# Optimization experiments

Measured on AMD Instinct MI355X. Metric: run time of the kernel, lower is better.

Reference implementation:

```python
import jax, jax.numpy as jnp
import numpy as np

M = 8          # ensemble size
B = 16384      # batch
HIST = 5       # history
L = 384        # latent_dim
A = 1          # action_dim
HID = 512      # hidden_dim
NHL = 2        # num_hidden_layers
DIN = L * HIST + A * HIST  # 1925
EPS = 1e-5     # BatchNorm eps


def setup_inputs() -> dict:
    key = jax.random.key(0)
    ks = jax.random.split(key, 6)
    w = lambda k, shape: (jax.random.normal(k, shape, jnp.float32) * 0.02)
    return {
        "z_hist": jax.random.normal(ks[0], (B, HIST, L), jnp.float32),
        "a_hist": jax.random.normal(ks[1], (B, HIST, A), jnp.float32),
        # per-model parameters, stacked along leading ensemble dim M
        "W1": w(ks[2], (M, DIN, HID)),
        "b1": jnp.zeros((M, HID), jnp.float32),
        "Wh": w(ks[3], (NHL, M, HID, HID)),
        "bh": jnp.zeros((NHL, M, HID), jnp.float32),
        "gamma": jnp.ones((NHL, M, HID), jnp.float32),
        "beta": jnp.zeros((NHL, M, HID), jnp.float32),
        "rmean": jnp.zeros((NHL, M, HID), jnp.float32),   # BN running mean (eval mode)
        "rvar": jnp.ones((NHL, M, HID), jnp.float32),      # BN running var (eval mode)
        "W3": w(ks[4], (M, HID, L)),
        "b3": jnp.zeros((M, L), jnp.float32),
    }


def reference(z_hist, a_hist, W1, b1, Wh, bh, gamma, beta, rmean, rvar, W3, b3):
    # EnsembleTransitionModel.forward, batched over the ensemble dim instead of
    # a Python loop over models. BatchNorm in eval mode; Dropout inactive (eval).
    bsz = z_hist.shape[0]
    x = jnp.concatenate([z_hist.reshape(bsz, -1), a_hist.reshape(bsz, -1)], axis=1)  # [B, DIN]
    # input projection + ReLU: [M, B, HID]
    h = jax.nn.relu(jnp.einsum('bi,mih->mbh', x, W1) + b1[:, None, :])
    n_layers = Wh.shape[0]
    for l in range(n_layers):  # small fixed structural loop (num_hidden_layers)
        h = jnp.einsum('mbh,mhk->mbk', h, Wh[l]) + bh[l][:, None, :]
        h = (h - rmean[l][:, None, :]) * jax.lax.rsqrt(rvar[l][:, None, :] + EPS)
        h = jax.nn.relu(h * gamma[l][:, None, :] + beta[l][:, None, :])
    delta = jnp.einsum('mbh,mhl->mbl', h, W3) + b3[:, None, :]
    # residual: pred_z = z_t + delta, broadcast over ensemble dim
    return delta + z_hist[:, -1, :][None, :, :]
```

## Files before the change

kernel.cpp:

```cpp
#include <hip/hip_runtime.h>
#include <hip/hip_bf16.h>

#define M_ENS 8
#define BATCH 16384
#define HIST 5
#define LDIM 384
#define HID 512
#define NHL 2
#define DIN 1925
#define KP 2048

typedef unsigned short u16;
typedef unsigned int u32;
typedef __attribute__((ext_vector_type(8))) short bf16x8;
typedef __attribute__((ext_vector_type(4))) float f32x4;

__device__ __forceinline__ u16 f2b(float f) {
    u32 u = __builtin_bit_cast(u32, f);
    u32 r = (u + 0x7fffu + ((u >> 16) & 1u)) >> 16;
    return (u16)r;
}

__global__ void build_x(const float* __restrict__ z, const float* __restrict__ a,
                        u16* __restrict__ xp) {
    int idx = blockIdx.x * 256 + threadIdx.x;
    int b = idx / (KP / 2);
    int k2 = (idx % (KP / 2)) * 2;
    if (b >= BATCH) return;
    u32 packed = 0;
#pragma unroll
    for (int j = 0; j < 2; ++j) {
        int k = k2 + j;
        float v = 0.f;
        if (k < HIST * LDIM) v = z[(size_t)b * (HIST * LDIM) + k];
        else if (k < DIN)    v = a[b * HIST + (k - HIST * LDIM)];
        packed |= ((u32)f2b(v)) << (16 * j);
    }
    *(u32*)(&xp[(size_t)b * KP + k2]) = packed;
}

__global__ void transpose_cvt(const float* __restrict__ in, u16* __restrict__ out,
                              int R, int C, int Rp) {
    __shared__ float tile[32][33];
    const float* inb = in + (size_t)blockIdx.z * R * C;
    u16* outb = out + (size_t)blockIdx.z * C * Rp;
    int r0 = blockIdx.x * 32, c0 = blockIdx.y * 32;
    int tx = threadIdx.x & 31, ty = threadIdx.x >> 5;
#pragma unroll
    for (int i = 0; i < 32; i += 8) {
        int r = r0 + ty + i;
        float v = 0.f;
        if (r < R) v = inb[(size_t)r * C + c0 + tx];
        tile[ty + i][tx] = v;
    }
    __syncthreads();
#pragma unroll
    for (int i = 0; i < 32; i += 8) {
        outb[(size_t)(c0 + ty + i) * Rp + r0 + tx] = f2b(tile[tx][ty + i]);
    }
}

__global__ void make_tables(const float* __restrict__ bh, const float* __restrict__ gamma,
                            const float* __restrict__ beta, const float* __restrict__ rmean,
                            const float* __restrict__ rvar, float* __restrict__ s,
                            float* __restrict__ t, int n) {
    int i = blockIdx.x * 256 + threadIdx.x;
    if (i >= n) return;
    float inv = rsqrtf(rvar[i] + 1e-5f);
    float sc = gamma[i] * inv;
    s[i] = sc;
    t[i] = (bh[i] - rmean[i]) * sc + beta[i];
}

#define BARRIER asm volatile("s_barrier" ::: "memory")

template <int MODE>
__global__ __launch_bounds__(512, 2) void gemm8p(
    const u16* __restrict__ A, const u16* __restrict__ Bw,
    const float* __restrict__ Sv, const float* __restrict__ Tv,
    u16* __restrict__ Ho, int K) {
    extern __shared__ char smem[];
    const int tid = threadIdx.x;
    const int lane = tid & 63;
    const int wid = tid >> 6;
    const int wm = wid >> 2;
    const int wn = wid & 3;

    const int nwg = gridDim.x;
    const int swz = (blockIdx.x & 7) * (nwg >> 3) + (blockIdx.x >> 3);

    int rowT, colT, mI;
    const u16 *Ab, *Bb;
    int lda, ldb;
    if (MODE == 0) {
        rowT = swz >> 4; colT = swz & 15;
        Ab = A; lda = KP;
        Bb = Bw + (size_t)colT * 256 * KP; ldb = KP;
        mI = 0;
    } else {
        mI = swz >> 7;
        int rem = swz & 127;
        rowT = rem >> 1; colT = rem & 1;
        Ab = A + (size_t)mI * BATCH * HID; lda = HID;
        Bb = Bw + (size_t)mI * HID * HID + (size_t)colT * 256 * HID; ldb = HID;
    }
    const int rowBase = rowT * 256;
    const int NT = K >> 6;

    auto STAGE = [&](int par, int op, int half, int tk) {
#pragma unroll
        for (int i = 0; i < 2; ++i) {
            int ii = wid * 2 + i;
            int row = ii * 8 + (lane >> 3);
            int gc = lane & 7;
            const u16* src;
            if (op == 0)
                src = Ab + (size_t)(rowBase + half * 128 + row) * lda + tk * 64 + ((gc ^ (row & 7)) << 3);
            else
                src = Bb + (size_t)(half * 128 + row) * ldb + tk * 64 + ((gc ^ (row & 7)) << 3);
            u16* dst = (u16*)(smem + par * 65536 + op * 32768 + half * 16384) + (size_t)(ii * 64 + lane) * 8;
            __builtin_amdgcn_global_load_lds((const __attribute__((address_space(1))) void*)src,
                                             (__attribute__((address_space(3))) void*)dst, 16, 0, 0);
        }
    };

    const int laneRow = lane & 15;
    int xg[2];
    xg[0] = (((lane >> 4)) ^ (lane & 7)) << 4;
    xg[1] = ((4 | (lane >> 4)) ^ (lane & 7)) << 4;
#define RDF(base, r, kk) (*(const bf16x8*)((base) + (size_t)(r) * 128 + xg[kk]))

    f32x4 acc[8][4] = {};
    bf16x8 af[4][2], bfr[4][2];
    const int bcol0 = (wn & 1) * 64;

    STAGE(0, 1, 0, 0); STAGE(0, 1, 1, 0);
    STAGE(0, 0, 0, 0); STAGE(0, 0, 1, 0);
    if (NT > 1) { STAGE(1, 1, 0, 1); STAGE(1, 1, 1, 1); }
    asm volatile("s_waitcnt vmcnt(4)" ::: "memory");
    BARRIER;

    for (int T = 0; T < NT; ++T) {
        const int p = T & 1;
        const char* pA = smem + p * 65536 + wm * 16384;
        const char* pB = smem + p * 65536 + 32768 + (wn >> 1) * 16384;

#pragma unroll
        for (int mf = 0; mf < 4; ++mf) {
            af[mf][0] = RDF(pA, mf * 16 + laneRow, 0);
            af[mf][1] = RDF(pA, mf * 16 + laneRow, 1);
        }
#pragma unroll
        for (int nf = 0; nf < 2; ++nf) {
            bfr[nf][0] = RDF(pB, bcol0 + nf * 16 + laneRow, 0);
            bfr[nf][1] = RDF(pB, bcol0 + nf * 16 + laneRow, 1);
        }
        if (T + 1 < NT) STAGE((T + 1) & 1, 0, 0, T + 1);
        BARRIER;
        __builtin_amdgcn_s_setprio(1);
#pragma unroll
        for (int kk = 0; kk < 2; ++kk)
#pragma unroll
            for (int mf = 0; mf < 4; ++mf)
#pragma unroll
                for (int nf = 0; nf < 2; ++nf)
                    acc[mf][nf] = __builtin_amdgcn_mfma_f32_16x16x32_bf16(af[mf][kk], bfr[nf][kk], acc[mf][nf], 0, 0, 0);
        __builtin_amdgcn_s_setprio(0);
        BARRIER;

#pragma unroll
        for (int nf = 2; nf < 4; ++nf) {
            bfr[nf][0] = RDF(pB, bcol0 + nf * 16 + laneRow, 0);
            bfr[nf][1] = RDF(pB, bcol0 + nf * 16 + laneRow, 1);
        }
        if (T + 1 < NT) STAGE((T + 1) & 1, 0, 1, T + 1);
        BARRIER;
        __builtin_amdgcn_s_setprio(1);
#pragma unroll
        for (int kk = 0; kk < 2; ++kk)
#pragma unroll
            for (int mf = 0; mf < 4; ++mf)
#pragma unroll
                for (int nf = 2; nf < 4; ++nf)
                    acc[mf][nf] = __builtin_amdgcn_mfma_f32_16x16x32_bf16(af[mf][kk], bfr[nf][kk], acc[mf][nf], 0, 0, 0);
        __builtin_amdgcn_s_setprio(0);
        BARRIER;

#pragma unroll
        for (int mf = 0; mf < 4; ++mf) {
            af[mf][0] = RDF(pA, (4 + mf) * 16 + laneRow, 0);
            af[mf][1] = RDF(pA, (4 + mf) * 16 + laneRow, 1);
        }
        if (T + 2 < NT) STAGE(p, 1, 0, T + 2);
        BARRIER;
        __builtin_amdgcn_s_setprio(1);
#pragma unroll
        for (int kk = 0; kk < 2; ++kk)
#pragma unroll
            for (int mf = 0; mf < 4; ++mf)
#pragma unroll
                for (int nf = 2; nf < 4; ++nf)
                    acc[4 + mf][nf] = __builtin_amdgcn_mfma_f32_16x16x32_bf16(af[mf][kk], bfr[nf][kk], acc[4 + mf][nf], 0, 0, 0);
        __builtin_amdgcn_s_setprio(0);
        BARRIER;

        if (T + 2 < NT) {
            STAGE(p, 1, 1, T + 2);
            asm volatile("s_waitcnt vmcnt(4)" ::: "memory");
        } else {
            asm volatile("s_waitcnt vmcnt(0)" ::: "memory");
        }
        BARRIER;
        __builtin_amdgcn_s_setprio(1);
#pragma unroll
        for (int kk = 0; kk < 2; ++kk)
#pragma unroll
            for (int mf = 0; mf < 4; ++mf)
#pragma unroll
                for (int nf = 0; nf < 2; ++nf)
                    acc[4 + mf][nf] = __builtin_amdgcn_mfma_f32_16x16x32_bf16(af[mf][kk], bfr[nf][kk], acc[4 + mf][nf], 0, 0, 0);
        __builtin_amdgcn_s_setprio(0);
        BARRIER;
    }

#pragma unroll
    for (int mf = 0; mf < 8; ++mf) {
        int row = rowBase + wm * 128 + mf * 16 + ((lane >> 4) << 2);
#pragma unroll
        for (int nf = 0; nf < 4; ++nf) {
            int c = colT * 256 + wn * 64 + nf * 16 + (lane & 15);
            if (MODE == 0) {
                float tb = Tv[c];
                size_t base = (size_t)(c >> 9) * BATCH * HID + (c & 511);
#pragma unroll
                for (int q = 0; q < 4; ++q) {
                    float v = acc[mf][nf][q] + tb;
                    Ho[base + (size_t)(row + q) * HID] = f2b(v > 0.f ? v : 0.f);
                }
            } else {
                float sc = Sv[mI * HID + c], tb = Tv[mI * HID + c];
                u16* H = Ho + (size_t)mI * BATCH * HID;
#pragma unroll
                for (int q = 0; q < 4; ++q) {
                    float v = acc[mf][nf][q] * sc + tb;
                    H[(size_t)(row + q) * HID + c] = f2b(v > 0.f ? v : 0.f);
                }
            }
        }
    }
}

template <int MODE>
__global__ __launch_bounds__(256, 2) void gemm_bt(
    const u16* __restrict__ A, size_t aStride, int lda,
    const u16* __restrict__ Bt, size_t bStride,
    const float* __restrict__ Sv, const float* __restrict__ Tv, int ptStride,
    u16* __restrict__ Ho, size_t hStride,
    float* __restrict__ Fo, size_t fStride,
    const float* __restrict__ Zres,
    int K, int m0) {
    __shared__ u16 As[128 * 64];
    __shared__ u16 Bs[128 * 64];

    const int tid = threadIdx.x;
    const int lane = tid & 63;
    const int wid = tid >> 6;
    const int wr = (wid >> 1) * 64;
    const int wc = (wid & 1) * 64;
    const int z = blockIdx.z;
    const int rowBase = blockIdx.x * 128;
    const int colBase = blockIdx.y * 128;

    const u16* Ab = A + (size_t)z * aStride;
    const u16* Bb = Bt + (size_t)z * bStride;

    f32x4 acc[4][4] = {};

    int aoff[4], boff[4];
#pragma unroll
    for (int f = 0; f < 4; ++f) {
        int ar = wr + f * 16 + (lane & 15);
        aoff[f] = (ar * 128 + ((lane >> 4) * 16)) ^ ((ar & 7) << 4);
        int br = wc + f * 16 + (lane & 15);
        boff[f] = (br * 128 + ((lane >> 4) * 16)) ^ ((br & 7) << 4);
    }

    for (int k0 = 0; k0 < K; k0 += 64) {
#pragma unroll
        for (int i = 0; i < 4; ++i) {
            int gg = i * 256 + tid;
            int row = gg >> 3, gc = gg & 7;
            const u16* srcA = Ab + (size_t)(rowBase + row) * lda + k0 + ((gc ^ (row & 7)) << 3);
            __builtin_amdgcn_global_load_lds(
                (const __attribute__((address_space(1))) void*)srcA,
                (__attribute__((address_space(3))) void*)(As + gg * 8), 16, 0, 0);
            const u16* srcB = Bb + (size_t)(colBase + row) * K + k0 + ((gc ^ (row & 7)) << 3);
            __builtin_amdgcn_global_load_lds(
                (const __attribute__((address_space(1))) void*)srcB,
                (__attribute__((address_space(3))) void*)(Bs + gg * 8), 16, 0, 0);
        }
        __syncthreads();
#pragma unroll
        for (int kk = 0; kk < 2; ++kk) {
            bf16x8 af[4], bfr[4];
#pragma unroll
            for (int f = 0; f < 4; ++f) {
                af[f]  = *(const bf16x8*)((const char*)As + (aoff[f] ^ (kk << 6)));
                bfr[f] = *(const bf16x8*)((const char*)Bs + (boff[f] ^ (kk << 6)));
            }
#pragma unroll
            for (int i = 0; i < 4; ++i)
#pragma unroll
                for (int j = 0; j < 4; ++j)
                    acc[i][j] = __builtin_amdgcn_mfma_f32_16x16x32_bf16(af[i], bfr[j], acc[i][j], 0, 0, 0);
        }
        __syncthreads();
    }

    const int mg = m0 + z;
#pragma unroll
    for (int i = 0; i < 4; ++i) {
        int rbase = rowBase + wr + i * 16 + ((lane >> 4) << 2);
#pragma unroll
        for (int j = 0; j < 4; ++j) {
            int n = colBase + wc + j * 16 + (lane & 15);
            if (MODE == 0) {
                float bias = Tv[(size_t)mg * ptStride + n];
                u16* H = Ho + (size_t)z * hStride;
#pragma unroll
                for (int q = 0; q < 4; ++q) {
                    float v = acc[i][j][q] + bias;
                    v = v > 0.f ? v : 0.f;
                    H[(size_t)(rbase + q) * HID + n] = f2b(v);
                }
            } else if (MODE == 1) {
                float sc = Sv[(size_t)mg * ptStride + n];
                float tt = Tv[(size_t)mg * ptStride + n];
                u16* H = Ho + (size_t)z * hStride;
#pragma unroll
                for (int q = 0; q < 4; ++q) {
                    float v = acc[i][j][q] * sc + tt;
                    v = v > 0.f ? v : 0.f;
                    H[(size_t)(rbase + q) * HID + n] = f2b(v);
                }
            } else {
                float bias = Tv[(size_t)mg * ptStride + n];
                float* F = Fo + (size_t)z * fStride;
#pragma unroll
                for (int q = 0; q < 4; ++q) {
                    int b = rbase + q;
                    float v = acc[i][j][q] + bias + Zres[(size_t)b * (HIST * LDIM) + (HIST - 1) * LDIM + n];
                    F[(size_t)b * LDIM + n] = v;
                }
            }
        }
    }
}

extern "C" void kernel_launch(void* const* d_in, const int* in_sizes, int n_in,
                              void* d_out, int out_size, void* d_ws, size_t ws_size,
                              hipStream_t stream) {
    const float* z_hist = (const float*)d_in[0];
    const float* a_hist = (const float*)d_in[1];
    const float* W1    = (const float*)d_in[2];
    const float* b1    = (const float*)d_in[3];
    const float* Wh    = (const float*)d_in[4];
    const float* bh    = (const float*)d_in[5];
    const float* gamma = (const float*)d_in[6];
    const float* beta  = (const float*)d_in[7];
    const float* rmean = (const float*)d_in[8];
    const float* rvar  = (const float*)d_in[9];
    const float* W3    = (const float*)d_in[10];
    const float* b3    = (const float*)d_in[11];
    float* out = (float*)d_out;

    char* ws = (char*)d_ws;
    size_t off = 0;
    auto alloc = [&](size_t bytes) {
        void* p = ws + off;
        off = (off + bytes + 255) & ~(size_t)255;
        return p;
    };
    u16* xp  = (u16*)alloc((size_t)BATCH * KP * 2);
    u16* W1t = (u16*)alloc((size_t)M_ENS * HID * KP * 2);
    u16* Wht = (u16*)alloc((size_t)NHL * M_ENS * HID * HID * 2);
    u16* W3t = (u16*)alloc((size_t)M_ENS * LDIM * HID * 2);
    float* stab = (float*)alloc((size_t)NHL * M_ENS * HID * 4);
    float* ttab = (float*)alloc((size_t)NHL * M_ENS * HID * 4);
    size_t fixed = off;
    size_t hFull = (size_t)M_ENS * BATCH * HID * 2;
    bool full = (fixed + 2 * hFull <= ws_size);
    int MC = full ? M_ENS : 1;
    u16* h0 = (u16*)alloc((size_t)MC * BATCH * HID * 2);
    u16* h1 = (u16*)alloc((size_t)MC * BATCH * HID * 2);

    {
        int total = BATCH * KP / 2;
        build_x<<<(total + 255) / 256, 256, 0, stream>>>(z_hist, a_hist, xp);
        dim3 g1(KP / 32, HID / 32, M_ENS);
        transpose_cvt<<<g1, 256, 0, stream>>>(W1, W1t, DIN, HID, KP);
        dim3 g2(HID / 32, HID / 32, NHL * M_ENS);
        transpose_cvt<<<g2, 256, 0, stream>>>(Wh, Wht, HID, HID, HID);
        dim3 g3(HID / 32, LDIM / 32, M_ENS);
        transpose_cvt<<<g3, 256, 0, stream>>>(W3, W3t, HID, LDIM, HID);
        int n = NHL * M_ENS * HID;
        make_tables<<<(n + 255) / 256, 256, 0, stream>>>(bh, gamma, beta, rmean, rvar, stab, ttab, n);
    }

    if (full) {
        (void)hipFuncSetAttribute(reinterpret_cast<const void*>(&gemm8p<0>),
                                  hipFuncAttributeMaxDynamicSharedMemorySize, 131072);
        (void)hipFuncSetAttribute(reinterpret_cast<const void*>(&gemm8p<1>),
                                  hipFuncAttributeMaxDynamicSharedMemorySize, 131072);
        gemm8p<0><<<1024, 512, 131072, stream>>>(xp, W1t, nullptr, b1, h0, KP);
        gemm8p<1><<<1024, 512, 131072, stream>>>(h0, Wht, stab, ttab, h1, HID);
        gemm8p<1><<<1024, 512, 131072, stream>>>(h1, Wht + (size_t)M_ENS * HID * HID,
                                                 stab + M_ENS * HID, ttab + M_ENS * HID, h0, HID);
        dim3 gridO(BATCH / 128, LDIM / 128, M_ENS);
        gemm_bt<2><<<gridO, 256, 0, stream>>>(
            h0, (size_t)BATCH * HID, HID,
            W3t, (size_t)LDIM * HID,
            nullptr, b3, LDIM,
            nullptr, 0,
            out, (size_t)BATCH * LDIM,
            z_hist,
            HID, 0);
    } else {
        for (int m0 = 0; m0 < M_ENS; m0 += MC) {
            dim3 grid(BATCH / 128, HID / 128, MC);
            gemm_bt<0><<<grid, 256, 0, stream>>>(
                xp, 0, KP,
                W1t + (size_t)m0 * HID * KP, (size_t)HID * KP,
                nullptr, b1, HID,
                h0, (size_t)BATCH * HID, nullptr, 0, nullptr,
                KP, m0);
            for (int l = 0; l < NHL; ++l) {
                u16* hin = l ? h1 : h0;
                u16* hout = l ? h0 : h1;
                gemm_bt<1><<<grid, 256, 0, stream>>>(
                    hin, (size_t)BATCH * HID, HID,
                    Wht + ((size_t)l * M_ENS + m0) * HID * HID, (size_t)HID * HID,
                    stab + (size_t)l * M_ENS * HID, ttab + (size_t)l * M_ENS * HID, HID,
                    hout, (size_t)BATCH * HID, nullptr, 0, nullptr,
                    HID, m0);
            }
            dim3 gridO(BATCH / 128, LDIM / 128, MC);
            gemm_bt<2><<<gridO, 256, 0, stream>>>(
                h0, (size_t)BATCH * HID, HID,
                W3t + (size_t)m0 * LDIM * HID, (size_t)LDIM * HID,
                nullptr, b3, LDIM,
                nullptr, 0,
                out + (size_t)m0 * BATCH * LDIM, (size_t)BATCH * LDIM,
                z_hist,
                HID, 0);
        }
    }
}
```

Baseline: 634.7 us.

## Fuse last hidden layer with output projection and remap W1 GEMM tiles per XCD

Adds a kernel h2out that computes the second hidden layer for a 128-row tile across all 512 columns, applies BN+ReLU, keeps the result in LDS, then multiplies by W3 and adds the bias and residual. This removes the bf16 h0 round trip through global memory and one launch. It also changes the first GEMM's block-to-tile mapping so each XCD handles a fixed pair of weight column tiles, which should improve L2 reuse. The fused kernel uses 160KB of LDS at one block per CU, so occupancy is lower, and the W3 stage reloads weights through a small LDS buffer with a barrier per step.

```diff
diff --git a/kernel.cpp b/kernel.cpp
--- a/kernel.cpp
+++ b/kernel.cpp
@@ -20,6 +20,8 @@
     u32 r = (u + 0x7fffu + ((u >> 16) & 1u)) >> 16;
     return (u16)r;
 }
+
+#define BARRIER asm volatile("s_barrier" ::: "memory")
 
 __global__ void build_x(const float* __restrict__ z, const float* __restrict__ a,
                         u16* __restrict__ xp) {
@@ -71,8 +73,6 @@
     s[i] = sc;
     t[i] = (bh[i] - rmean[i]) * sc + beta[i];
 }
-
-#define BARRIER asm volatile("s_barrier" ::: "memory")
 
 template <int MODE>
 __global__ __launch_bounds__(512, 2) void gemm8p(
@@ -86,18 +86,18 @@
     const int wm = wid >> 2;
     const int wn = wid & 3;
 
-    const int nwg = gridDim.x;
-    const int swz = (blockIdx.x & 7) * (nwg >> 3) + (blockIdx.x >> 3);
-
     int rowT, colT, mI;
     const u16 *Ab, *Bb;
     int lda, ldb;
     if (MODE == 0) {
-        rowT = swz >> 4; colT = swz & 15;
+        int xcd = blockIdx.x & 7, i = blockIdx.x >> 3;
+        rowT = i >> 1; colT = xcd * 2 + (i & 1);
         Ab = A; lda = KP;
         Bb = Bw + (size_t)colT * 256 * KP; ldb = KP;
         mI = 0;
     } else {
+        const int nwg = gridDim.x;
+        const int swz = (blockIdx.x & 7) * (nwg >> 3) + (blockIdx.x >> 3);
         mI = swz >> 7;
         int rem = swz & 127;
         rowT = rem >> 1; colT = rem & 1;
@@ -245,6 +245,230 @@
                     float v = acc[mf][nf][q] * sc + tb;
                     H[(size_t)(row + q) * HID + c] = f2b(v > 0.f ? v : 0.f);
                 }
+            }
+        }
+    }
+}
+
+__global__ __launch_bounds__(512, 1) void h2out(
+    const u16* __restrict__ h1, const u16* __restrict__ Wh2,
+    const float* __restrict__ Sv, const float* __restrict__ Tv,
+    const u16* __restrict__ W3p, const float* __restrict__ b3,
+    const float* __restrict__ zres, float* __restrict__ out) {
+    extern __shared__ char smem[];
+    const int tid = threadIdx.x;
+    const int lane = tid & 63;
+    const int wid = tid >> 6;
+    const int wm = wid >> 2;
+    const int wn = wid & 3;
+    const int m = blockIdx.x & 7;
+    const int rowBase = (blockIdx.x >> 3) * 128;
+    const int lr15 = lane & 15;
+
+    const u16* Ab = h1 + ((size_t)m * BATCH + rowBase) * HID;
+    const u16* Bb = Wh2 + (size_t)m * HID * HID;
+    const u16* W3b = W3p + (size_t)m * LDIM * HID;
+    const float* b3b = b3 + m * LDIM;
+
+    int xg[2];
+    xg[0] = (((lane >> 4)) ^ (lane & 7)) << 4;
+    xg[1] = ((4 | (lane >> 4)) ^ (lane & 7)) << 4;
+
+    auto stA = [&](int par, int tk) {
+#pragma unroll
+        for (int i = 0; i < 2; ++i) {
+            int ii = wid * 2 + i;
+            int row = ii * 8 + (lane >> 3);
+            int gc = lane & 7;
+            const u16* src = Ab + (size_t)row * HID + tk * 64 + ((gc ^ (row & 7)) << 3);
+            u16* dst = (u16*)(smem + par * 16384) + (size_t)(ii * 64 + lane) * 8;
+            __builtin_amdgcn_global_load_lds((const __attribute__((address_space(1))) void*)src,
+                                             (__attribute__((address_space(3))) void*)dst, 16, 0, 0);
+        }
+    };
+    auto stB = [&](int par, int q, int tk) {
+#pragma unroll
+        for (int i = 0; i < 2; ++i) {
+            int ii = wid * 2 + i;
+            int row = ii * 8 + (lane >> 3);
+            int gc = lane & 7;
+            const u16* src = Bb + (size_t)(q * 128 + row) * HID + tk * 64 + ((gc ^ (row & 7)) << 3);
+            u16* dst = (u16*)(smem + 32768 + par * 65536 + q * 16384) + (size_t)(ii * 64 + lane) * 8;
+            __builtin_amdgcn_global_load_lds((const __attribute__((address_space(1))) void*)src,
+                                             (__attribute__((address_space(3))) void*)dst, 16, 0, 0);
+        }
+    };
+
+    f32x4 acc[4][8] = {};
+    bf16x8 afr[4][2];
+    const int NT = HID / 64;
+
+    stA(0, 0); stB(0, 0, 0); stB(0, 1, 0); stB(0, 2, 0); stB(0, 3, 0);
+    asm volatile("s_waitcnt vmcnt(0)" ::: "memory");
+    BARRIER;
+
+    for (int T = 0; T < NT; ++T) {
+        const int p = T & 1;
+        const char* pA = smem + p * 16384;
+        const char* qb = smem + 32768 + p * 65536 + wn * 16384;
+
+#pragma unroll
+        for (int mf = 0; mf < 4; ++mf) {
+            int lr = wm * 64 + mf * 16 + lr15;
+            afr[mf][0] = RDF(pA, lr, 0);
+            afr[mf][1] = RDF(pA, lr, 1);
+        }
+        bf16x8 b01[2][2];
+#pragma unroll
+        for (int nf = 0; nf < 2; ++nf) {
+            b01[nf][0] = RDF(qb, nf * 16 + lr15, 0);
+            b01[nf][1] = RDF(qb, nf * 16 + lr15, 1);
+        }
+        if (T + 1 < NT) stA(p ^ 1, T + 1);
+        BARRIER;
+        __builtin_amdgcn_s_setprio(1);
+#pragma unroll
+        for (int kk = 0; kk < 2; ++kk)
+#pragma unroll
+            for (int mf = 0; mf < 4; ++mf)
+#pragma unroll
+                for (int nf = 0; nf < 2; ++nf)
+                    acc[mf][nf] = __builtin_amdgcn_mfma_f32_16x16x32_bf16(afr[mf][kk], b01[nf][kk], acc[mf][nf], 0, 0, 0);
+        __builtin_amdgcn_s_setprio(0);
+        BARRIER;
+
+#pragma unroll
+        for (int nf = 0; nf < 2; ++nf) {
+            b01[nf][0] = RDF(qb, (2 + nf) * 16 + lr15, 0);
+            b01[nf][1] = RDF(qb, (2 + nf) * 16 + lr15, 1);
+        }
+        if (T + 1 < NT) { stB(p ^ 1, 0, T + 1); stB(p ^ 1, 1, T + 1); }
+        BARRIER;
+        __builtin_amdgcn_s_setprio(1);
+#pragma unroll
+        for (int kk = 0; kk < 2; ++kk)
+#pragma unroll
+            for (int mf = 0; mf < 4; ++mf)
+#pragma unroll
+                for (int nf = 0; nf < 2; ++nf)
+                    acc[mf][2 + nf] = __builtin_amdgcn_mfma_f32_16x16x32_bf16(afr[mf][kk], b01[nf][kk], acc[mf][2 + nf], 0, 0, 0);
+        __builtin_amdgcn_s_setprio(0);
+        BARRIER;
+
+#pragma unroll
+        for (int nf = 0; nf < 2; ++nf) {
+            b01[nf][0] = RDF(qb, (4 + nf) * 16 + lr15, 0);
+            b01[nf][1] = RDF(qb, (4 + nf) * 16 + lr15, 1);
+        }
+        if (T + 1 < NT) { stB(p ^ 1, 2, T + 1); stB(p ^ 1, 3, T + 1); }
+        BARRIER;
+        __builtin_amdgcn_s_setprio(1);
+#pragma unroll
+        for (int kk = 0; kk < 2; ++kk)
+#pragma unroll
+            for (int mf = 0; mf < 4; ++mf)
+#pragma unroll
+                for (int nf = 0; nf < 2; ++nf)
+                    acc[mf][4 + nf] = __builtin_amdgcn_mfma_f32_16x16x32_bf16(afr[mf][kk], b01[nf][kk], acc[mf][4 + nf], 0, 0, 0);
+        __builtin_amdgcn_s_setprio(0);
+        BARRIER;
+
+#pragma unroll
+        for (int nf = 0; nf < 2; ++nf) {
+            b01[nf][0] = RDF(qb, (6 + nf) * 16 + lr15, 0);
+            b01[nf][1] = RDF(qb, (6 + nf) * 16 + lr15, 1);
+        }
+        if (T + 2 < NT) {
+            stA(p, T + 2);
+            asm volatile("s_waitcnt vmcnt(2)" ::: "memory");
+        } else {
+            asm volatile("s_waitcnt vmcnt(0)" ::: "memory");
+        }
+        BARRIER;
+        __builtin_amdgcn_s_setprio(1);
+#pragma unroll
+        for (int kk = 0; kk < 2; ++kk)
+#pragma unroll
+            for (int mf = 0; mf < 4; ++mf)
+#pragma unroll
+                for (int nf = 0; nf < 2; ++nf)
+                    acc[mf][6 + nf] = __builtin_amdgcn_mfma_f32_16x16x32_bf16(afr[mf][kk], b01[nf][kk], acc[mf][6 + nf], 0, 0, 0);
+        __builtin_amdgcn_s_setprio(0);
+        BARRIER;
+    }
+
+#pragma unroll
+    for (int mf = 0; mf < 4; ++mf) {
+#pragma unroll
+        for (int nf = 0; nf < 8; ++nf) {
+            int col = wn * 128 + nf * 16 + lr15;
+            float sc = Sv[m * HID + col], tt = Tv[m * HID + col];
+#pragma unroll
+            for (int q = 0; q < 4; ++q) {
+                int row = wm * 64 + mf * 16 + ((lane >> 4) << 2) + q;
+                float v = acc[mf][nf][q] * sc + tt;
+                v = v > 0.f ? v : 0.f;
+                *(u16*)(smem + 32768 + row * 1024 + (((col >> 3) ^ (row & 7)) << 4) + ((col & 7) << 1)) = f2b(v);
+            }
+        }
+    }
+    asm volatile("s_waitcnt lgkmcnt(0)" ::: "memory");
+    BARRIER;
+
+    bf16x8 w3r[3];
+#pragma unroll
+    for (int j = 0; j < 3; ++j) {
+        int gi = tid * 3 + j;
+        w3r[j] = *(const bf16x8*)(W3b + (size_t)(gi >> 2) * HID + ((gi & 3) << 3));
+    }
+    f32x4 acc2[4][6] = {};
+    for (int t = 0; t < 16; ++t) {
+#pragma unroll
+        for (int j = 0; j < 3; ++j) {
+            int gi = tid * 3 + j;
+            *(bf16x8*)(smem + (gi >> 2) * 64 + (((gi & 3) ^ ((gi >> 2) & 3)) << 4)) = w3r[j];
+        }
+        if (t + 1 < 16) {
+#pragma unroll
+            for (int j = 0; j < 3; ++j) {
+                int gi = tid * 3 + j;
+                w3r[j] = *(const bf16x8*)(W3b + (size_t)(gi >> 2) * HID + (t + 1) * 32 + ((gi & 3) << 3));
+            }
+        }
+        asm volatile("s_waitcnt lgkmcnt(0)" ::: "memory");
+        BARRIER;
+        bf16x8 a1[4], b1r[6];
+#pragma unroll
+        for (int mf = 0; mf < 4; ++mf) {
+            int r = wm * 64 + mf * 16 + lr15;
+            a1[mf] = *(const bf16x8*)(smem + 32768 + r * 1024 + (((4 * t + (lane >> 4)) ^ (lane & 7)) << 4));
+        }
+#pragma unroll
+        for (int nf = 0; nf < 6; ++nf) {
+            int r3 = wn * 96 + nf * 16 + lr15;
+            b1r[nf] = *(const bf16x8*)(smem + r3 * 64 + (((lane >> 4) ^ (r3 & 3)) << 4));
+        }
+        __builtin_amdgcn_s_setprio(1);
+#pragma unroll
+        for (int mf = 0; mf < 4; ++mf)
+#pragma unroll
+            for (int nf = 0; nf < 6; ++nf)
+                acc2[mf][nf] = __builtin_amdgcn_mfma_f32_16x16x32_bf16(a1[mf], b1r[nf], acc2[mf][nf], 0, 0, 0);
+        __builtin_amdgcn_s_setprio(0);
+        BARRIER;
+    }
+
+#pragma unroll
+    for (int mf = 0; mf < 4; ++mf) {
+#pragma unroll
+        for (int nf = 0; nf < 6; ++nf) {
+            int c = wn * 96 + nf * 16 + lr15;
+            float bv = b3b[c];
+#pragma unroll
+            for (int q = 0; q < 4; ++q) {
+                int grow = rowBase + wm * 64 + mf * 16 + ((lane >> 4) << 2) + q;
+                out[((size_t)m * BATCH + grow) * LDIM + c] =
+                    acc2[mf][nf][q] + bv + zres[(size_t)grow * (HIST * LDIM) + (HIST - 1) * LDIM + c];
             }
         }
     }
@@ -412,19 +636,14 @@
                                   hipFuncAttributeMaxDynamicSharedMemorySize, 131072);
         (void)hipFuncSetAttribute(reinterpret_cast<const void*>(&gemm8p<1>),
                                   hipFuncAttributeMaxDynamicSharedMemorySize, 131072);
+        (void)hipFuncSetAttribute(reinterpret_cast<const void*>(&h2out),
+                                  hipFuncAttributeMaxDynamicSharedMemorySize, 163840);
         gemm8p<0><<<1024, 512, 131072, stream>>>(xp, W1t, nullptr, b1, h0, KP);
         gemm8p<1><<<1024, 512, 131072, stream>>>(h0, Wht, stab, ttab, h1, HID);
-        gemm8p<1><<<1024, 512, 131072, stream>>>(h1, Wht + (size_t)M_ENS * HID * HID,
-                                                 stab + M_ENS * HID, ttab + M_ENS * HID, h0, HID);
-        dim3 gridO(BATCH / 128, LDIM / 128, M_ENS);
-        gemm_bt<2><<<gridO, 256, 0, stream>>>(
-            h0, (size_t)BATCH * HID, HID,
-            W3t, (size_t)LDIM * HID,
-            nullptr, b3, LDIM,
-            nullptr, 0,
-            out, (size_t)BATCH * LDIM,
-            z_hist,
-            HID, 0);
+        h2out<<<1024, 512, 163840, stream>>>(
+            h1, Wht + (size_t)M_ENS * HID * HID,
+            stab + M_ENS * HID, ttab + M_ENS * HID,
+            W3t, b3, z_hist, out);
     } else {
         for (int m0 = 0; m0 < M_ENS; m0 += MC) {
             dim3 grid(BATCH / 128, HID / 128, MC);
@@ -452,7 +671,7 @@
                 nullptr, 0,
                 out + (size_t)m0 * BATCH * LDIM, (size_t)BATCH * LDIM,
                 z_hist,
-                HID, 0);
-        }
-    }
-}
+                HID, m0);
+        }
+    }
+}
```

After: 626.5 us. No clear change (-1.3%).

## Fuse whole MLP chain into one persistent-tile kernel keeping activations in LDS

Applied to the files above, without the earlier changes.

Replaces the four separate GEMM launches (input projection, two hidden layers, output projection) with one fused kernel. Each workgroup owns a 128-row batch tile for one ensemble member and keeps the 128x512 hidden activation in LDS across layers. Weights for the hidden and output layers are streamed through a small LDS buffer in 32-wide K chunks, with the next chunk prefetched into registers. This removes the global write and reread of the large bf16 intermediate activations and three launches. In exchange it uses 160KB LDS with one block per CU, and the later layers use simple single-buffered weight streaming with many barriers, which may lower MFMA utilisation. Each block also re-reads the full weights per layer, increasing weight traffic.

```diff
diff --git a/kernel.cpp b/kernel.cpp
--- a/kernel.cpp
+++ b/kernel.cpp
@@ -20,6 +20,11 @@
     u32 r = (u + 0x7fffu + ((u >> 16) & 1u)) >> 16;
     return (u16)r;
 }
+
+#define BARRIER asm volatile("s_barrier" ::: "memory")
+#define GLL(src, dst) __builtin_amdgcn_global_load_lds( \
+    (const __attribute__((address_space(1))) void*)(src), \
+    (__attribute__((address_space(3))) void*)(dst), 16, 0, 0)
 
 __global__ void build_x(const float* __restrict__ z, const float* __restrict__ a,
                         u16* __restrict__ xp) {
@@ -72,178 +77,270 @@
     t[i] = (bh[i] - rmean[i]) * sc + beta[i];
 }
 
-#define BARRIER asm volatile("s_barrier" ::: "memory")
-
-template <int MODE>
-__global__ __launch_bounds__(512, 2) void gemm8p(
-    const u16* __restrict__ A, const u16* __restrict__ Bw,
-    const float* __restrict__ Sv, const float* __restrict__ Tv,
-    u16* __restrict__ Ho, int K) {
+__global__ __launch_bounds__(512, 1) void fused_all(
+    const u16* __restrict__ xp, const u16* __restrict__ W1t,
+    const float* __restrict__ b1,
+    const u16* __restrict__ Wht, const float* __restrict__ stab,
+    const float* __restrict__ ttab,
+    const u16* __restrict__ W3t, const float* __restrict__ b3,
+    const float* __restrict__ zres, float* __restrict__ out) {
     extern __shared__ char smem[];
     const int tid = threadIdx.x;
     const int lane = tid & 63;
     const int wid = tid >> 6;
     const int wm = wid >> 2;
     const int wn = wid & 3;
-
-    const int nwg = gridDim.x;
-    const int swz = (blockIdx.x & 7) * (nwg >> 3) + (blockIdx.x >> 3);
-
-    int rowT, colT, mI;
-    const u16 *Ab, *Bb;
-    int lda, ldb;
-    if (MODE == 0) {
-        rowT = swz >> 4; colT = swz & 15;
-        Ab = A; lda = KP;
-        Bb = Bw + (size_t)colT * 256 * KP; ldb = KP;
-        mI = 0;
-    } else {
-        mI = swz >> 7;
-        int rem = swz & 127;
-        rowT = rem >> 1; colT = rem & 1;
-        Ab = A + (size_t)mI * BATCH * HID; lda = HID;
-        Bb = Bw + (size_t)mI * HID * HID + (size_t)colT * 256 * HID; ldb = HID;
-    }
-    const int rowBase = rowT * 256;
-    const int NT = K >> 6;
-
-    auto STAGE = [&](int par, int op, int half, int tk) {
-#pragma unroll
-        for (int i = 0; i < 2; ++i) {
-            int ii = wid * 2 + i;
-            int row = ii * 8 + (lane >> 3);
-            int gc = lane & 7;
-            const u16* src;
-            if (op == 0)
-                src = Ab + (size_t)(rowBase + half * 128 + row) * lda + tk * 64 + ((gc ^ (row & 7)) << 3);
-            else
-                src = Bb + (size_t)(half * 128 + row) * ldb + tk * 64 + ((gc ^ (row & 7)) << 3);
-            u16* dst = (u16*)(smem + par * 65536 + op * 32768 + half * 16384) + (size_t)(ii * 64 + lane) * 8;
-            __builtin_amdgcn_global_load_lds((const __attribute__((address_space(1))) void*)src,
-                                             (__attribute__((address_space(3))) void*)dst, 16, 0, 0);
-        }
-    };
-
-    const int laneRow = lane & 15;
+    const int lr15 = lane & 15;
+    const int m = blockIdx.x & 7;
+    const int rowBase = (blockIdx.x >> 3) * 128;
+
+    const u16* Ab = xp + (size_t)rowBase * KP;
+    const u16* Bb = W1t + (size_t)m * HID * KP;
+
     int xg[2];
     xg[0] = (((lane >> 4)) ^ (lane & 7)) << 4;
     xg[1] = ((4 | (lane >> 4)) ^ (lane & 7)) << 4;
 #define RDF(base, r, kk) (*(const bf16x8*)((base) + (size_t)(r) * 128 + xg[kk]))
 
-    f32x4 acc[8][4] = {};
-    bf16x8 af[4][2], bfr[4][2];
-    const int bcol0 = (wn & 1) * 64;
-
-    STAGE(0, 1, 0, 0); STAGE(0, 1, 1, 0);
-    STAGE(0, 0, 0, 0); STAGE(0, 0, 1, 0);
-    if (NT > 1) { STAGE(1, 1, 0, 1); STAGE(1, 1, 1, 1); }
-    asm volatile("s_waitcnt vmcnt(4)" ::: "memory");
-    BARRIER;
-
-    for (int T = 0; T < NT; ++T) {
-        const int p = T & 1;
-        const char* pA = smem + p * 65536 + wm * 16384;
-        const char* pB = smem + p * 65536 + 32768 + (wn >> 1) * 16384;
+    auto stA0 = [&](int par, int tk) {
+#pragma unroll
+        for (int i = 0; i < 2; ++i) {
+            int gg = i * 512 + tid;
+            int row = gg >> 3, gc = gg & 7;
+            const u16* src = Ab + (size_t)row * KP + tk * 64 + ((gc ^ (row & 7)) << 3);
+            GLL(src, (u16*)(smem + par * 16384) + gg * 8);
+        }
+    };
+    auto stB0 = [&](int par, int half, int tk) {
+#pragma unroll
+        for (int i = 0; i < 4; ++i) {
+            int gg = i * 512 + tid;
+            int row = half * 256 + (gg >> 3), gc = gg & 7;
+            const u16* src = Bb + (size_t)row * KP + tk * 64 + ((gc ^ (row & 7)) << 3);
+            GLL(src, (u16*)(smem + 32768 + par * 65536 + half * 32768) + gg * 8);
+        }
+    };
+
+    f32x4 acc[4][8] = {};
+
+    {
+        const int NT = KP >> 6;
+        stA0(0, 0); stB0(0, 0, 0); stB0(0, 1, 0); stA0(1, 1);
+        asm volatile("s_waitcnt vmcnt(2)" ::: "memory");
+        BARRIER;
+
+        for (int T = 0; T < NT; ++T) {
+            const int p = T & 1;
+            const char* pA = smem + p * 16384;
+            const char* pB = smem + 32768 + p * 65536;
+            bf16x8 af[4][2], bfrA[4], bfrB[4];
+
+#pragma unroll
+            for (int mf = 0; mf < 4; ++mf) af[mf][0] = RDF(pA, wm * 64 + mf * 16 + lr15, 0);
+#pragma unroll
+            for (int nf = 0; nf < 4; ++nf) bfrA[nf] = RDF(pB, wn * 128 + nf * 16 + lr15, 0);
+            if (T + 1 < NT) stB0(p ^ 1, 0, T + 1);
+            BARRIER;
+            __builtin_amdgcn_s_setprio(1);
+#pragma unroll
+            for (int mf = 0; mf < 4; ++mf)
+#pragma unroll
+                for (int nf = 0; nf < 4; ++nf)
+                    acc[mf][nf] = __builtin_amdgcn_mfma_f32_16x16x32_bf16(af[mf][0], bfrA[nf], acc[mf][nf], 0, 0, 0);
+            __builtin_amdgcn_s_setprio(0);
+            BARRIER;
+
+#pragma unroll
+            for (int mf = 0; mf < 4; ++mf) af[mf][1] = RDF(pA, wm * 64 + mf * 16 + lr15, 1);
+#pragma unroll
+            for (int nf = 0; nf < 4; ++nf) bfrB[nf] = RDF(pB, wn * 128 + (4 + nf) * 16 + lr15, 0);
+            if (T + 1 < NT) stB0(p ^ 1, 1, T + 1);
+            asm volatile("s_waitcnt lgkmcnt(0)" ::: "memory");
+            BARRIER;
+            __builtin_amdgcn_s_setprio(1);
+#pragma unroll
+            for (int mf = 0; mf < 4; ++mf)
+#pragma unroll
+                for (int nf = 0; nf < 4; ++nf)
+                    acc[mf][4 + nf] = __builtin_amdgcn_mfma_f32_16x16x32_bf16(af[mf][0], bfrB[nf], acc[mf][4 + nf], 0, 0, 0);
+            __builtin_amdgcn_s_setprio(0);
+            BARRIER;
+
+#pragma unroll
+            for (int nf = 0; nf < 4; ++nf) bfrA[nf] = RDF(pB, wn * 128 + nf * 16 + lr15, 1);
+            if (T + 2 < NT) stA0(p, T + 2);
+            BARRIER;
+            __builtin_amdgcn_s_setprio(1);
+#pragma unroll
+            for (int mf = 0; mf < 4; ++mf)
+#pragma unroll
+                for (int nf = 0; nf < 4; ++nf)
+                    acc[mf][nf] = __builtin_amdgcn_mfma_f32_16x16x32_bf16(af[mf][1], bfrA[nf], acc[mf][nf], 0, 0, 0);
+            __builtin_amdgcn_s_setprio(0);
+            BARRIER;
+
+#pragma unroll
+            for (int nf = 0; nf < 4; ++nf) bfrB[nf] = RDF(pB, wn * 128 + (4 + nf) * 16 + lr15, 1);
+            if (T + 2 < NT) {
+                asm volatile("s_waitcnt vmcnt(2)" ::: "memory");
+            } else {
+                asm volatile("s_waitcnt vmcnt(0)" ::: "memory");
+            }
+            BARRIER;
+            __builtin_amdgcn_s_setprio(1);
+#pragma unroll
+            for (int mf = 0; mf < 4; ++mf)
+#pragma unroll
+                for (int nf = 0; nf < 4; ++nf)
+                    acc[mf][4 + nf] = __builtin_amdgcn_mfma_f32_16x16x32_bf16(af[mf][1], bfrB[nf], acc[mf][4 + nf], 0, 0, 0);
+            __builtin_amdgcn_s_setprio(0);
+            BARRIER;
+        }
 
 #pragma unroll
         for (int mf = 0; mf < 4; ++mf) {
-            af[mf][0] = RDF(pA, mf * 16 + laneRow, 0);
-            af[mf][1] = RDF(pA, mf * 16 + laneRow, 1);
-        }
-#pragma unroll
-        for (int nf = 0; nf < 2; ++nf) {
-            bfr[nf][0] = RDF(pB, bcol0 + nf * 16 + laneRow, 0);
-            bfr[nf][1] = RDF(pB, bcol0 + nf * 16 + laneRow, 1);
-        }
-        if (T + 1 < NT) STAGE((T + 1) & 1, 0, 0, T + 1);
+#pragma unroll
+            for (int nf = 0; nf < 8; ++nf) {
+                int col = wn * 128 + nf * 16 + lr15;
+                float tb = b1[m * HID + col];
+#pragma unroll
+                for (int q = 0; q < 4; ++q) {
+                    int row = wm * 64 + mf * 16 + ((lane >> 4) << 2) + q;
+                    float v = acc[mf][nf][q] + tb;
+                    v = v > 0.f ? v : 0.f;
+                    *(u16*)(smem + 32768 + row * 1024 + (((col >> 3) ^ (row & 7)) << 4) + ((col & 7) << 1)) = f2b(v);
+                }
+            }
+        }
+        asm volatile("s_waitcnt lgkmcnt(0)" ::: "memory");
         BARRIER;
-        __builtin_amdgcn_s_setprio(1);
-#pragma unroll
-        for (int kk = 0; kk < 2; ++kk)
+    }
+
+    for (int l = 0; l < NHL; ++l) {
+        const u16* Wl = Wht + ((size_t)l * M_ENS + m) * HID * HID;
+        const float* Sv = stab + ((size_t)l * M_ENS + m) * HID;
+        const float* Tv = ttab + ((size_t)l * M_ENS + m) * HID;
+#pragma unroll
+        for (int mf = 0; mf < 4; ++mf)
+#pragma unroll
+            for (int nf = 0; nf < 8; ++nf) acc[mf][nf] = (f32x4){0.f, 0.f, 0.f, 0.f};
+
+        bf16x8 w[4];
+#pragma unroll
+        for (int j = 0; j < 4; ++j) {
+            int gi = tid * 4 + j;
+            w[j] = *(const bf16x8*)(Wl + (size_t)(gi >> 2) * HID + ((gi & 3) << 3));
+        }
+        for (int t = 0; t < 16; ++t) {
+#pragma unroll
+            for (int j = 0; j < 4; ++j) {
+                int gi = tid * 4 + j;
+                *(bf16x8*)(smem + (gi >> 2) * 64 + (((gi & 3) ^ ((gi >> 2) & 3)) << 4)) = w[j];
+            }
+            if (t + 1 < 16) {
+#pragma unroll
+                for (int j = 0; j < 4; ++j) {
+                    int gi = tid * 4 + j;
+                    w[j] = *(const bf16x8*)(Wl + (size_t)(gi >> 2) * HID + (t + 1) * 32 + ((gi & 3) << 3));
+                }
+            }
+            asm volatile("s_waitcnt lgkmcnt(0)" ::: "memory");
+            BARRIER;
+            bf16x8 a1[4], b1r[8];
+#pragma unroll
+            for (int mf = 0; mf < 4; ++mf) {
+                int r = wm * 64 + mf * 16 + lr15;
+                a1[mf] = *(const bf16x8*)(smem + 32768 + r * 1024 + (((4 * t + (lane >> 4)) ^ (r & 7)) << 4));
+            }
+#pragma unroll
+            for (int nf = 0; nf < 8; ++nf) {
+                int c = wn * 128 + nf * 16 + lr15;
+                b1r[nf] = *(const bf16x8*)(smem + c * 64 + (((lane >> 4) ^ (c & 3)) << 4));
+            }
+            __builtin_amdgcn_s_setprio(1);
 #pragma unroll
             for (int mf = 0; mf < 4; ++mf)
 #pragma unroll
-                for (int nf = 0; nf < 2; ++nf)
-                    acc[mf][nf] = __builtin_amdgcn_mfma_f32_16x16x32_bf16(af[mf][kk], bfr[nf][kk], acc[mf][nf], 0, 0, 0);
-        __builtin_amdgcn_s_setprio(0);
+                for (int nf = 0; nf < 8; ++nf)
+                    acc[mf][nf] = __builtin_amdgcn_mfma_f32_16x16x32_bf16(a1[mf], b1r[nf], acc[mf][nf], 0, 0, 0);
+            __builtin_amdgcn_s_setprio(0);
+            BARRIER;
+        }
+#pragma unroll
+        for (int mf = 0; mf < 4; ++mf) {
+#pragma unroll
+            for (int nf = 0; nf < 8; ++nf) {
+                int col = wn * 128 + nf * 16 + lr15;
+                float sc = Sv[col], tt = Tv[col];
+#pragma unroll
+                for (int q = 0; q < 4; ++q) {
+                    int row = wm * 64 + mf * 16 + ((lane >> 4) << 2) + q;
+                    float v = acc[mf][nf][q] * sc + tt;
+                    v = v > 0.f ? v : 0.f;
+                    *(u16*)(smem + 32768 + row * 1024 + (((col >> 3) ^ (row & 7)) << 4) + ((col & 7) << 1)) = f2b(v);
+                }
+            }
+        }
+        asm volatile("s_waitcnt lgkmcnt(0)" ::: "memory");
         BARRIER;
-
-#pragma unroll
-        for (int nf = 2; nf < 4; ++nf) {
-            bfr[nf][0] = RDF(pB, bcol0 + nf * 16 + laneRow, 0);
-            bfr[nf][1] = RDF(pB, bcol0 + nf * 16 + laneRow, 1);
-        }
-        if (T + 1 < NT) STAGE((T + 1) & 1, 0, 1, T + 1);
-        BARRIER;
-        __builtin_amdgcn_s_setprio(1);
-#pragma unroll
-        for (int kk = 0; kk < 2; ++kk)
+    }
+
+    {
+        const u16* W3b = W3t + (size_t)m * LDIM * HID;
+        const float* b3b = b3 + m * LDIM;
+        bf16x8 w3r[3];
+#pragma unroll
+        for (int j = 0; j < 3; ++j) {
+            int gi = tid * 3 + j;
+            w3r[j] = *(const bf16x8*)(W3b + (size_t)(gi >> 2) * HID + ((gi & 3) << 3));
+        }
+        f32x4 acc2[4][6] = {};
+        for (int t = 0; t < 16; ++t) {
+#pragma unroll
+            for (int j = 0; j < 3; ++j) {
+                int gi = tid * 3 + j;
+                *(bf16x8*)(smem + (gi >> 2) * 64 + (((gi & 3) ^ ((gi >> 2) & 3)) << 4)) = w3r[j];
+            }
+            if (t + 1 < 16) {
+#pragma unroll
+                for (int j = 0; j < 3; ++j) {
+                    int gi = tid * 3 + j;
+                    w3r[j] = *(const bf16x8*)(W3b + (size_t)(gi >> 2) * HID + (t + 1) * 32 + ((gi & 3) << 3));
+                }
+            }
+            asm volatile("s_waitcnt lgkmcnt(0)" ::: "memory");
+            BARRIER;
+            bf16x8 a1[4], b1r[6];
+#pragma unroll
+            for (int mf = 0; mf < 4; ++mf) {
+                int r = wm * 64 + mf * 16 + lr15;
+                a1[mf] = *(const bf16x8*)(smem + 32768 + r * 1024 + (((4 * t + (lane >> 4)) ^ (r & 7)) << 4));
+            }
+#pragma unroll
+            for (int nf = 0; nf < 6; ++nf) {
+                int r3 = wn * 96 + nf * 16 + lr15;
+                b1r[nf] = *(const bf16x8*)(smem + r3 * 64 + (((lane >> 4) ^ (r3 & 3)) << 4));
+            }
+            __builtin_amdgcn_s_setprio(1);
 #pragma unroll
             for (int mf = 0; mf < 4; ++mf)
 #pragma unroll
-                for (int nf = 2; nf < 4; ++nf)
-                    acc[mf][nf] = __builtin_amdgcn_mfma_f32_16x16x32_bf16(af[mf][kk], bfr[nf][kk], acc[mf][nf], 0, 0, 0);
-        __builtin_amdgcn_s_setprio(0);
-        BARRIER;
-
+                for (int nf = 0; nf < 6; ++nf)
+                    acc2[mf][nf] = __builtin_amdgcn_mfma_f32_16x16x32_bf16(a1[mf], b1r[nf], acc2[mf][nf], 0, 0, 0);
+            __builtin_amdgcn_s_setprio(0);
+            BARRIER;
+        }
 #pragma unroll
         for (int mf = 0; mf < 4; ++mf) {
-            af[mf][0] = RDF(pA, (4 + mf) * 16 + laneRow, 0);
-            af[mf][1] = RDF(pA, (4 + mf) * 16 + laneRow, 1);
-        }
-        if (T + 2 < NT) STAGE(p, 1, 0, T + 2);
-        BARRIER;
-        __builtin_amdgcn_s_setprio(1);
-#pragma unroll
-        for (int kk = 0; kk < 2; ++kk)
-#pragma unroll
-            for (int mf = 0; mf < 4; ++mf)
-#pragma unroll
-                for (int nf = 2; nf < 4; ++nf)
-                    acc[4 + mf][nf] = __builtin_amdgcn_mfma_f32_16x16x32_bf16(af[mf][kk], bfr[nf][kk], acc[4 + mf][nf], 0, 0, 0);
-        __builtin_amdgcn_s_setprio(0);
-        BARRIER;
-
-        if (T + 2 < NT) {
-            STAGE(p, 1, 1, T + 2);
-            asm volatile("s_waitcnt vmcnt(4)" ::: "memory");
-        } else {
-            asm volatile("s_waitcnt vmcnt(0)" ::: "memory");
-        }
-        BARRIER;
-        __builtin_amdgcn_s_setprio(1);
-#pragma unroll
-        for (int kk = 0; kk < 2; ++kk)
-#pragma unroll
-            for (int mf = 0; mf < 4; ++mf)
-#pragma unroll
-                for (int nf = 0; nf < 2; ++nf)
-                    acc[4 + mf][nf] = __builtin_amdgcn_mfma_f32_16x16x32_bf16(af[mf][kk], bfr[nf][kk], acc[4 + mf][nf], 0, 0, 0);
-        __builtin_amdgcn_s_setprio(0);
-        BARRIER;
-    }
-
-#pragma unroll
-    for (int mf = 0; mf < 8; ++mf) {
-        int row = rowBase + wm * 128 + mf * 16 + ((lane >> 4) << 2);
-#pragma unroll
-        for (int nf = 0; nf < 4; ++nf) {
-            int c = colT * 256 + wn * 64 + nf * 16 + (lane & 15);
-            if (MODE == 0) {
-                float tb = Tv[c];
-                size_t base = (size_t)(c >> 9) * BATCH * HID + (c & 511);
+#pragma unroll
+            for (int nf = 0; nf < 6; ++nf) {
+                int c = wn * 96 + nf * 16 + lr15;
+                float bv = b3b[c];
 #pragma unroll
                 for (int q = 0; q < 4; ++q) {
-                    float v = acc[mf][nf][q] + tb;
-                    Ho[base + (size_t)(row + q) * HID] = f2b(v > 0.f ? v : 0.f);
-                }
-            } else {
-                float sc = Sv[mI * HID + c], tb = Tv[mI * HID + c];
-                u16* H = Ho + (size_t)mI * BATCH * HID;
-#pragma unroll
-                for (int q = 0; q < 4; ++q) {
-                    float v = acc[mf][nf][q] * sc + tb;
-                    H[(size_t)(row + q) * HID + c] = f2b(v > 0.f ? v : 0.f);
+                    int grow = rowBase + wm * 64 + mf * 16 + ((lane >> 4) << 2) + q;
+                    out[((size_t)m * BATCH + grow) * LDIM + c] =
+                        acc2[mf][nf][q] + bv + zres[(size_t)grow * (HIST * LDIM) + (HIST - 1) * LDIM + c];
                 }
             }
         }
@@ -291,13 +388,9 @@
             int gg = i * 256 + tid;
             int row = gg >> 3, gc = gg & 7;
             const u16* srcA = Ab + (size_t)(rowBase + row) * lda + k0 + ((gc ^ (row & 7)) << 3);
-            __builtin_amdgcn_global_load_lds(
-                (const __attribute__((address_space(1))) void*)srcA,
-                (__attribute__((address_space(3))) void*)(As + gg * 8), 16, 0, 0);
+            GLL(srcA, As + gg * 8);
             const u16* srcB = Bb + (size_t)(colBase + row) * K + k0 + ((gc ^ (row & 7)) << 3);
-            __builtin_amdgcn_global_load_lds(
-                (const __attribute__((address_space(1))) void*)srcB,
-                (__attribute__((address_space(3))) void*)(Bs + gg * 8), 16, 0, 0);
+            GLL(srcB, Bs + gg * 8);
         }
         __syncthreads();
 #pragma unroll
@@ -388,11 +481,11 @@
     float* stab = (float*)alloc((size_t)NHL * M_ENS * HID * 4);
     float* ttab = (float*)alloc((size_t)NHL * M_ENS * HID * 4);
     size_t fixed = off;
-    size_t hFull = (size_t)M_ENS * BATCH * HID * 2;
-    bool full = (fixed + 2 * hFull <= ws_size);
-    int MC = full ? M_ENS : 1;
-    u16* h0 = (u16*)alloc((size_t)MC * BATCH * HID * 2);
-    u16* h1 = (u16*)alloc((size_t)MC * BATCH * HID * 2);
+    bool full = (fixed <= ws_size);
+    size_t hFull = (size_t)BATCH * HID * 2;
+    bool fitsFallback = (fixed + 2 * hFull <= ws_size);
+    u16* h0 = (u16*)alloc(hFull);
+    u16* h1 = (u16*)alloc(hFull);
 
     {
         int total = BATCH * KP / 2;
@@ -408,26 +501,13 @@
     }
 
     if (full) {
-        (void)hipFuncSetAttribute(reinterpret_cast<const void*>(&gemm8p<0>),
-                                  hipFuncAttributeMaxDynamicSharedMemorySize, 131072);
-        (void)hipFuncSetAttribute(reinterpret_cast<const void*>(&gemm8p<1>),
-                                  hipFuncAttributeMaxDynamicSharedMemorySize, 131072);
-        gemm8p<0><<<1024, 512, 131072, stream>>>(xp, W1t, nullptr, b1, h0, KP);
-        gemm8p<1><<<1024, 512, 131072, stream>>>(h0, Wht, stab, ttab, h1, HID);
-        gemm8p<1><<<1024, 512, 131072, stream>>>(h1, Wht + (size_t)M_ENS * HID * HID,
-                                                 stab + M_ENS * HID, ttab + M_ENS * HID, h0, HID);
-        dim3 gridO(BATCH / 128, LDIM / 128, M_ENS);
-        gemm_bt<2><<<gridO, 256, 0, stream>>>(
-            h0, (size_t)BATCH * HID, HID,
-            W3t, (size_t)LDIM * HID,
-            nullptr, b3, LDIM,
-            nullptr, 0,
-            out, (size_t)BATCH * LDIM,
-            z_hist,
-            HID, 0);
-    } else {
-        for (int m0 = 0; m0 < M_ENS; m0 += MC) {
-            dim3 grid(BATCH / 128, HID / 128, MC);
+        (void)hipFuncSetAttribute(reinterpret_cast<const void*>(&fused_all),
+                                  hipFuncAttributeMaxDynamicSharedMemorySize, 163840);
+        fused_all<<<1024, 512, 163840, stream>>>(
+            xp, W1t, b1, Wht, stab, ttab, W3t, b3, z_hist, out);
+    } else if (fitsFallback) {
+        for (int m0 = 0; m0 < M_ENS; ++m0) {
+            dim3 grid(BATCH / 128, HID / 128, 1);
             gemm_bt<0><<<grid, 256, 0, stream>>>(
                 xp, 0, KP,
                 W1t + (size_t)m0 * HID * KP, (size_t)HID * KP,
@@ -444,7 +524,7 @@
                     hout, (size_t)BATCH * HID, nullptr, 0, nullptr,
                     HID, m0);
             }
-            dim3 gridO(BATCH / 128, LDIM / 128, MC);
+            dim3 gridO(BATCH / 128, LDIM / 128, 1);
             gemm_bt<2><<<gridO, 256, 0, stream>>>(
                 h0, (size_t)BATCH * HID, HID,
                 W3t + (size_t)m0 * LDIM * HID, (size_t)LDIM * HID,
```

After: 923.5 us. 45.5% more time.
